# Performance work log

Hardware: AMD Instinct MI355X
Metric: run time of the kernel (lower is better)

The kernel has to match this reference:

```python
import jax, jax.numpy as jnp
import numpy as np

HEADS = 4
OUT_DIM = 64
NEG_SLOPE = 0.2


def setup_inputs() -> dict:
    key = jax.random.key(0)
    k1, k2, k3, k4 = jax.random.split(key, 4)
    n, in_dim = 4096, 256
    x = jax.random.normal(k1, (n, in_dim), dtype=jnp.float32)
    adj = jax.random.randint(k2, (n, n), 0, 2, dtype=jnp.int32)
    # lin: in_dim -> heads*out_dim (no bias), stored as [in_dim, heads*out_dim]
    W = jax.random.normal(k3, (in_dim, HEADS * OUT_DIM), dtype=jnp.float32) * 0.05
    # att_weight: [heads, 2*out_dim]
    att = jax.random.normal(k4, (HEADS, 2 * OUT_DIM), dtype=jnp.float32) * 0.05
    return {"x": x, "adj": adj, "W": W, "att": att}


def reference(x, adj, W, att):
    n = x.shape[0]
    h = (x @ W).reshape(n, HEADS, OUT_DIM)  # [n, H, D]
    # scores[i,j,h] = att[h] . cat(h_i, h_j) = <h_i, a_src[h]> + <h_j, a_dst[h]>
    a_src, a_dst = att[:, :OUT_DIM], att[:, OUT_DIM:]
    e_src = jnp.einsum('nhd,hd->nh', h, a_src)  # [n, H]
    e_dst = jnp.einsum('nhd,hd->nh', h, a_dst)  # [n, H]
    scores = e_src[:, None, :] + e_dst[None, :, :]  # [n, n, H]
    scores = jax.nn.leaky_relu(scores, negative_slope=NEG_SLOPE)
    mask = (adj > 0)[:, :, None]  # [n, n, 1]
    scores = jnp.where(mask, scores, -jnp.inf)
    alpha = jax.nn.softmax(scores, axis=1)  # softmax over neighbors j
    # h_prime[i,h,d] = sum_j alpha[i,j,h] * h[j,h,d]
    h_prime = jnp.einsum('ijh,jhd->ihd', alpha, h)
    return h_prime.reshape(n, HEADS * OUT_DIM)
```

## Files before the change

### kernel.cpp

```cpp
#include <hip/hip_runtime.h>
#include <hip/hip_bf16.h>

#define HEADS 4
#define ODIM 64
#define HD 256
#define NEG_SLOPE 0.2f

typedef __attribute__((ext_vector_type(8))) short bf16x8;
typedef __attribute__((ext_vector_type(4))) float floatx4;
typedef __attribute__((ext_vector_type(2))) float floatx2;

__global__ __launch_bounds__(256) void pack_xw(const float* __restrict__ x,
                                               const float* __restrict__ W,
                                               __hip_bfloat16* __restrict__ xh,
                                               __hip_bfloat16* __restrict__ xl,
                                               __hip_bfloat16* __restrict__ wh,
                                               __hip_bfloat16* __restrict__ wl,
                                               int K, int nxb) {
    const int b = blockIdx.x;
    const int Kc = K >> 5;
    if (b < nxb) {
        const int g = b * 256 + threadIdx.x;
        const int lane = g & 63, frag = g >> 6;
        const int kc = frag % Kc, mc = frag / Kc;
        const int l16 = lane & 15, q = lane >> 4;
        const float* src = x + (size_t)(mc * 16 + l16) * K + kc * 32 + q * 8;
        const float4 v0 = *(const float4*)src;
        const float4 v1 = *(const float4*)(src + 4);
        const float vv[8] = {v0.x, v0.y, v0.z, v0.w, v1.x, v1.y, v1.z, v1.w};
        union { __hip_bfloat16 b[8]; bf16x8 v; } H, L;
        #pragma unroll
        for (int p = 0; p < 8; ++p) {
            H.b[p] = __float2bfloat16(vv[p]);
            L.b[p] = __float2bfloat16(vv[p] - __bfloat162float(H.b[p]));
        }
        *(bf16x8*)&xh[(size_t)frag * 512 + lane * 8] = H.v;
        *(bf16x8*)&xl[(size_t)frag * 512 + lane * 8] = L.v;
    } else {
        const int g = (b - nxb) * 256 + threadIdx.x;
        const int lane = g & 63, frag = g >> 6;
        const int kc = frag % Kc, nc = frag / Kc;
        const int l16 = lane & 15, q = lane >> 4;
        union { __hip_bfloat16 b[8]; bf16x8 v; } H, L;
        #pragma unroll
        for (int p = 0; p < 8; ++p) {
            const float w = W[(size_t)(kc * 32 + q * 8 + p) * HD + nc * 16 + l16];
            H.b[p] = __float2bfloat16(w);
            L.b[p] = __float2bfloat16(w - __bfloat162float(H.b[p]));
        }
        *(bf16x8*)&wh[(size_t)frag * 512 + lane * 8] = H.v;
        *(bf16x8*)&wl[(size_t)frag * 512 + lane * 8] = L.v;
    }
}

__global__ __launch_bounds__(256) void gemm_fused(
    const __hip_bfloat16* __restrict__ xh, const __hip_bfloat16* __restrict__ xl,
    const __hip_bfloat16* __restrict__ wh, const __hip_bfloat16* __restrict__ wl,
    const float* __restrict__ att, float4* __restrict__ E4,
    __hip_bfloat16* __restrict__ hbB, int n, int K) {

    __shared__ __hip_bfloat16 T[64][80];

    const int tid = threadIdx.x, wave = tid >> 6, lane = tid & 63;
    const int q = lane >> 4, l16 = lane & 15;
    const int m0 = blockIdx.x * 64;
    const int head = blockIdx.y;
    const int Kc = K >> 5;
    const int mc = (m0 >> 4) + wave;

    floatx4 acc[4] = {{0.f,0.f,0.f,0.f},{0.f,0.f,0.f,0.f},{0.f,0.f,0.f,0.f},{0.f,0.f,0.f,0.f}};

    const __hip_bfloat16* Axh = xh + (size_t)mc * Kc * 512 + lane * 8;
    const __hip_bfloat16* Axl = xl + (size_t)mc * Kc * 512 + lane * 8;
    const __hip_bfloat16* Bwh = wh + lane * 8;
    const __hip_bfloat16* Bwl = wl + lane * 8;
    #pragma unroll 2
    for (int kc = 0; kc < Kc; ++kc) {
        const bf16x8 ah = *(const bf16x8*)(Axh + (size_t)kc * 512);
        const bf16x8 al = *(const bf16x8*)(Axl + (size_t)kc * 512);
        #pragma unroll
        for (int nt = 0; nt < 4; ++nt) {
            const size_t fo = (size_t)((head * 4 + nt) * Kc + kc) * 512;
            const bf16x8 bh = *(const bf16x8*)(Bwh + fo);
            const bf16x8 bl = *(const bf16x8*)(Bwl + fo);
            acc[nt] = __builtin_amdgcn_mfma_f32_16x16x32_bf16(ah, bh, acc[nt], 0, 0, 0);
            acc[nt] = __builtin_amdgcn_mfma_f32_16x16x32_bf16(ah, bl, acc[nt], 0, 0, 0);
            acc[nt] = __builtin_amdgcn_mfma_f32_16x16x32_bf16(al, bh, acc[nt], 0, 0, 0);
        }
    }

    float as_v[4], ad_v[4];
    #pragma unroll
    for (int nt = 0; nt < 4; ++nt) {
        as_v[nt] = att[head * 2 * ODIM + nt * 16 + l16];
        ad_v[nt] = att[head * 2 * ODIM + ODIM + nt * 16 + l16];
    }
    #pragma unroll
    for (int r = 0; r < 4; ++r) {
        float ps = 0.f, pd = 0.f;
        #pragma unroll
        for (int nt = 0; nt < 4; ++nt) {
            ps = fmaf(acc[nt][r], as_v[nt], ps);
            pd = fmaf(acc[nt][r], ad_v[nt], pd);
        }
        #pragma unroll
        for (int m = 1; m <= 8; m <<= 1) {
            ps += __shfl_xor(ps, m, 64);
            pd += __shfl_xor(pd, m, 64);
        }
        if (l16 == 0) {
            const int i = m0 + wave * 16 + q * 4 + r;
            E4[i * HEADS + head] = make_float4(__expf(ps), __expf(NEG_SLOPE * ps),
                                               __expf(pd), __expf(NEG_SLOPE * pd));
        }
    }

    #pragma unroll
    for (int nt = 0; nt < 4; ++nt) {
        union { __hip_bfloat16 b[4]; uint2 u; } pk;
        #pragma unroll
        for (int r = 0; r < 4; ++r) pk.b[r] = __float2bfloat16(acc[nt][r]);
        *(uint2*)&T[nt * 16 + l16][wave * 16 + q * 4] = pk.u;
    }
    __syncthreads();

    #pragma unroll
    for (int ffi = 0; ffi < 2; ++ffi) {
        const int ff = (tid >> 6) + ffi * 4;
        const int kcl = ff >> 2, nt = ff & 3;
        const bf16x8 v = *(const bf16x8*)&T[nt * 16 + l16][kcl * 32 + q * 8];
        const size_t frag = ((size_t)head * (n >> 5) + (m0 >> 5) + kcl) * 4 + nt;
        *(bf16x8*)&hbB[frag * 512 + lane * 8] = v;
    }
}

__global__ __launch_bounds__(256, 4) void aggregate(
    const int* __restrict__ adj, const float4* __restrict__ E4,
    const __hip_bfloat16* __restrict__ hbB, float* __restrict__ outsp,
    float* __restrict__ densp, int n, int KR) {

    __shared__ unsigned short adjL[2][32][72];
    __shared__ float2 EdL[2][HEADS][64];

    const int tid = threadIdx.x;
    const int wave = tid >> 6, lane = tid & 63;
    const int q = lane >> 4, l16 = lane & 15, q8 = (lane >> 4) * 8;
    const int i0 = blockIdx.x * 32;
    const int K0 = blockIdx.y * KR;

    const int sr = tid >> 3, sg = (tid & 7) * 8;
    const int je = tid >> 2, he = tid & 3;

    floatx2 es12[2];
    #pragma unroll
    for (int mt = 0; mt < 2; ++mt) {
        const float4 e = E4[(i0 + mt * 16 + l16) * HEADS + wave];
        es12[mt][0] = e.x; es12[mt][1] = e.y;
    }

    union { short s[8]; bf16x8 v; } bones;
    #pragma unroll
    for (int p = 0; p < 8; ++p) bones.s[p] = (l16 == 0) ? (short)0x3F80 : (short)0;

    floatx4 acc[2][4];
    floatx4 accd[2];
    #pragma unroll
    for (int mt = 0; mt < 2; ++mt) {
        accd[mt] = (floatx4){0.f, 0.f, 0.f, 0.f};
        #pragma unroll
        for (int nt = 0; nt < 4; ++nt) acc[mt][nt] = (floatx4){0.f, 0.f, 0.f, 0.f};
    }

    const int* aprow = &adj[(size_t)(i0 + sr) * n];

    int4 aj0, aj1; float4 ev;
    {
        const int* ap = aprow + K0 + sg;
        aj0 = *(const int4*)ap; aj1 = *(const int4*)(ap + 4);
        ev = E4[(K0 + je) * HEADS + he];
    }
    auto stage = [&](int buf) {
        const int av[8] = {aj0.x, aj0.y, aj0.z, aj0.w, aj1.x, aj1.y, aj1.z, aj1.w};
        uint4 u;
        u.x = (av[0] > 0 ? 0xFFFFu : 0u) | (av[1] > 0 ? 0xFFFF0000u : 0u);
        u.y = (av[2] > 0 ? 0xFFFFu : 0u) | (av[3] > 0 ? 0xFFFF0000u : 0u);
        u.z = (av[4] > 0 ? 0xFFFFu : 0u) | (av[5] > 0 ? 0xFFFF0000u : 0u);
        u.w = (av[6] > 0 ? 0xFFFFu : 0u) | (av[7] > 0 ? 0xFFFF0000u : 0u);
        *(uint4*)&adjL[buf][sr][sg] = u;
        EdL[buf][he][je] = make_float2(ev.z, ev.w);
    };
    stage(0);
    __syncthreads();

    int cur = 0;
    for (int jc = K0; jc < K0 + KR; jc += 64) {
        int jn = jc + 64; if (jn >= K0 + KR) jn = K0;
        {
            const int* ap = aprow + jn + sg;
            aj0 = *(const int4*)ap; aj1 = *(const int4*)(ap + 4);
            ev = E4[(jn + je) * HEADS + he];
        }

        const size_t kbase = ((size_t)wave * (n >> 5) + (jc >> 5)) * 4;
        #pragma unroll
        for (int ks = 0; ks < 2; ++ks) {
            bf16x8 bfr[4];
            #pragma unroll
            for (int nt = 0; nt < 4; ++nt)
                bfr[nt] = *(const bf16x8*)&hbB[(kbase + ks * 4 + nt) * 512 + lane * 8];

            const float4* ep = (const float4*)&EdL[cur][wave][ks * 32 + q8];
            const float4 e01 = ep[0], e23 = ep[1], e45 = ep[2], e67 = ep[3];
            floatx2 ed[8];
            ed[0][0]=e01.x; ed[0][1]=e01.y;  ed[1][0]=e01.z; ed[1][1]=e01.w;
            ed[2][0]=e23.x; ed[2][1]=e23.y;  ed[3][0]=e23.z; ed[3][1]=e23.w;
            ed[4][0]=e45.x; ed[4][1]=e45.y;  ed[5][0]=e45.z; ed[5][1]=e45.w;
            ed[6][0]=e67.x; ed[6][1]=e67.y;  ed[7][0]=e67.z; ed[7][1]=e67.w;

            #pragma unroll
            for (int mt = 0; mt < 2; ++mt) {
                const uint4 msk = *(const uint4*)&adjL[cur][mt * 16 + l16][ks * 32 + q8];
                const unsigned int mm[4] = {msk.x, msk.y, msk.z, msk.w};
                union { unsigned int u[4]; bf16x8 v; } af;
                #pragma unroll
                for (int p = 0; p < 4; ++p) {
                    const floatx2 pa = es12[mt] * ed[2 * p];
                    const floatx2 pb = es12[mt] * ed[2 * p + 1];
                    const float wa = fmaxf(pa[0], pa[1]);
                    const float wb = fmaxf(pb[0], pb[1]);
                    af.u[p] = __builtin_amdgcn_perm(__float_as_uint(wb), __float_as_uint(wa),
                                                    0x07060302u) & mm[p];
                }
                #pragma unroll
                for (int nt = 0; nt < 4; ++nt)
                    acc[mt][nt] = __builtin_amdgcn_mfma_f32_16x16x32_bf16(af.v, bfr[nt], acc[mt][nt], 0, 0, 0);
                accd[mt] = __builtin_amdgcn_mfma_f32_16x16x32_bf16(af.v, bones.v, accd[mt], 0, 0, 0);
            }
        }

        stage(cur ^ 1);
        __syncthreads();
        cur ^= 1;
    }

    const size_t sOut = (size_t)blockIdx.y * n * HD;
    #pragma unroll
    for (int mt = 0; mt < 2; ++mt)
        #pragma unroll
        for (int nt = 0; nt < 4; ++nt)
            #pragma unroll
            for (int r = 0; r < 4; ++r)
                outsp[sOut + (size_t)(i0 + mt * 16 + q * 4 + r) * HD + wave * ODIM + nt * 16 + l16] = acc[mt][nt][r];
    if (l16 == 0) {
        #pragma unroll
        for (int mt = 0; mt < 2; ++mt)
            #pragma unroll
            for (int r = 0; r < 4; ++r)
                densp[((size_t)blockIdx.y * n + i0 + mt * 16 + q * 4 + r) * HEADS + wave] = accd[mt][r];
    }
}

__global__ __launch_bounds__(256) void normalize(const float* __restrict__ outsp,
                                                 const float* __restrict__ densp,
                                                 float* __restrict__ out, int n, int splits) {
    const int g = blockIdx.x * 256 + threadIdx.x;
    const int i = g >> 6;
    const int c4 = (g & 63) * 4;
    const int head = c4 >> 6;
    float den = 0.f;
    for (int s = 0; s < splits; ++s) den += densp[((size_t)s * n + i) * HEADS + head];
    float4 v = {0.f, 0.f, 0.f, 0.f};
    for (int s = 0; s < splits; ++s) {
        const float4 t = *(const float4*)&outsp[(size_t)s * n * HD + (size_t)i * HD + c4];
        v.x += t.x; v.y += t.y; v.z += t.z; v.w += t.w;
    }
    const float inv = 1.0f / den;
    v.x *= inv; v.y *= inv; v.z *= inv; v.w *= inv;
    *(float4*)&out[(size_t)i * HD + c4] = v;
}

extern "C" void kernel_launch(void* const* d_in, const int* in_sizes, int n_in,
                              void* d_out, int out_size, void* d_ws, size_t ws_size,
                              hipStream_t stream) {
    const float* x   = (const float*)d_in[0];
    const int*   adj = (const int*)d_in[1];
    const float* W   = (const float*)d_in[2];
    const float* att = (const float*)d_in[3];
    float* out = (float*)d_out;

    const int in_dim = in_sizes[2] / HD;
    const int n = in_sizes[0] / in_dim;

    char* ws = (char*)d_ws;
    size_t off = 0;
    auto alloc = [&](size_t bytes) -> void* {
        void* p = ws + off; off += (bytes + 255) & ~(size_t)255; return p;
    };
    __hip_bfloat16* xh = (__hip_bfloat16*)alloc((size_t)n * in_dim * 2);
    __hip_bfloat16* xl = (__hip_bfloat16*)alloc((size_t)n * in_dim * 2);
    __hip_bfloat16* wh = (__hip_bfloat16*)alloc((size_t)in_dim * HD * 2);
    __hip_bfloat16* wl = (__hip_bfloat16*)alloc((size_t)in_dim * HD * 2);
    float4*         E4 = (float4*)alloc((size_t)n * HEADS * 16);
    __hip_bfloat16* hbB = (__hip_bfloat16*)alloc((size_t)n * HD * 2);

    const size_t outB = (size_t)n * HD * 4, denB = (size_t)n * HEADS * 4;
    int splits = 1;
    if      (ws_size >= off + 8 * (outB + denB)) splits = 8;
    else if (ws_size >= off + 4 * (outB + denB)) splits = 4;
    else if (ws_size >= off + 2 * (outB + denB)) splits = 2;
    float* densp = (float*)alloc((size_t)splits * denB);
    float* outsp = (splits == 1) ? out : (float*)alloc((size_t)splits * outB);

    const int nxb = (n / 16) * (in_dim / 32) * 64 / 256;
    const int nwb = (HD / 16) * (in_dim / 32) * 64 / 256;
    pack_xw<<<nxb + nwb, 256, 0, stream>>>(x, W, xh, xl, wh, wl, in_dim, nxb);
    gemm_fused<<<dim3(n / 64, HEADS), 256, 0, stream>>>(xh, xl, wh, wl, att, E4, hbB, n, in_dim);
    aggregate<<<dim3(n / 32, splits), 256, 0, stream>>>(adj, E4, hbB, outsp, densp, n, n / splits);
    normalize<<<n * 64 / 256, 256, 0, stream>>>(outsp, densp, out, n, splits);
}
```

Measured before the change: 147.4 us.

## Widen aggregate j-chunks to 128 with register double-prefetch and fixed 4 splits

After: 143.6 us. 2.6% less time.

```diff
diff --git a/kernel.cpp b/kernel.cpp
--- a/kernel.cpp
+++ b/kernel.cpp
@@ -5,6 +5,8 @@
 #define ODIM 64
 #define HD 256
 #define NEG_SLOPE 0.2f
+#define SPLITS 4
+#define BJ 128
 
 typedef __attribute__((ext_vector_type(8))) short bf16x8;
 typedef __attribute__((ext_vector_type(4))) float floatx4;
@@ -53,17 +55,17 @@
     }
 }
 
-__global__ __launch_bounds__(256) void gemm_fused(
+__global__ __launch_bounds__(128) void gemm_fused(
     const __hip_bfloat16* __restrict__ xh, const __hip_bfloat16* __restrict__ xl,
     const __hip_bfloat16* __restrict__ wh, const __hip_bfloat16* __restrict__ wl,
     const float* __restrict__ att, float4* __restrict__ E4,
     __hip_bfloat16* __restrict__ hbB, int n, int K) {
 
-    __shared__ __hip_bfloat16 T[64][80];
+    __shared__ __hip_bfloat16 T[64][40];
 
     const int tid = threadIdx.x, wave = tid >> 6, lane = tid & 63;
     const int q = lane >> 4, l16 = lane & 15;
-    const int m0 = blockIdx.x * 64;
+    const int m0 = blockIdx.x * 32;
     const int head = blockIdx.y;
     const int Kc = K >> 5;
     const int mc = (m0 >> 4) + wave;
@@ -78,15 +80,22 @@
     for (int kc = 0; kc < Kc; ++kc) {
         const bf16x8 ah = *(const bf16x8*)(Axh + (size_t)kc * 512);
         const bf16x8 al = *(const bf16x8*)(Axl + (size_t)kc * 512);
+        bf16x8 bh[4], bl[4];
         #pragma unroll
         for (int nt = 0; nt < 4; ++nt) {
             const size_t fo = (size_t)((head * 4 + nt) * Kc + kc) * 512;
-            const bf16x8 bh = *(const bf16x8*)(Bwh + fo);
-            const bf16x8 bl = *(const bf16x8*)(Bwl + fo);
-            acc[nt] = __builtin_amdgcn_mfma_f32_16x16x32_bf16(ah, bh, acc[nt], 0, 0, 0);
-            acc[nt] = __builtin_amdgcn_mfma_f32_16x16x32_bf16(ah, bl, acc[nt], 0, 0, 0);
-            acc[nt] = __builtin_amdgcn_mfma_f32_16x16x32_bf16(al, bh, acc[nt], 0, 0, 0);
-        }
+            bh[nt] = *(const bf16x8*)(Bwh + fo);
+            bl[nt] = *(const bf16x8*)(Bwl + fo);
+        }
+        #pragma unroll
+        for (int nt = 0; nt < 4; ++nt)
+            acc[nt] = __builtin_amdgcn_mfma_f32_16x16x32_bf16(ah, bh[nt], acc[nt], 0, 0, 0);
+        #pragma unroll
+        for (int nt = 0; nt < 4; ++nt)
+            acc[nt] = __builtin_amdgcn_mfma_f32_16x16x32_bf16(ah, bl[nt], acc[nt], 0, 0, 0);
+        #pragma unroll
+        for (int nt = 0; nt < 4; ++nt)
+            acc[nt] = __builtin_amdgcn_mfma_f32_16x16x32_bf16(al, bh[nt], acc[nt], 0, 0, 0);
     }
 
     float as_v[4], ad_v[4];
@@ -126,21 +135,20 @@
 
     #pragma unroll
     for (int ffi = 0; ffi < 2; ++ffi) {
-        const int ff = (tid >> 6) + ffi * 4;
-        const int kcl = ff >> 2, nt = ff & 3;
-        const bf16x8 v = *(const bf16x8*)&T[nt * 16 + l16][kcl * 32 + q * 8];
-        const size_t frag = ((size_t)head * (n >> 5) + (m0 >> 5) + kcl) * 4 + nt;
+        const int f = wave + ffi * 2;
+        const bf16x8 v = *(const bf16x8*)&T[f * 16 + l16][q * 8];
+        const size_t frag = ((size_t)head * (n >> 5) + (m0 >> 5)) * 4 + f;
         *(bf16x8*)&hbB[frag * 512 + lane * 8] = v;
     }
 }
 
-__global__ __launch_bounds__(256, 4) void aggregate(
+__global__ __launch_bounds__(256, 2) void aggregate(
     const int* __restrict__ adj, const float4* __restrict__ E4,
     const __hip_bfloat16* __restrict__ hbB, float* __restrict__ outsp,
     float* __restrict__ densp, int n, int KR) {
 
-    __shared__ unsigned short adjL[2][32][72];
-    __shared__ float2 EdL[2][HEADS][64];
+    __shared__ unsigned short adjL[2][32][136];
+    __shared__ float2 EdL[2][HEADS][BJ];
 
     const int tid = threadIdx.x;
     const int wave = tid >> 6, lane = tid & 63;
@@ -148,8 +156,8 @@
     const int i0 = blockIdx.x * 32;
     const int K0 = blockIdx.y * KR;
 
-    const int sr = tid >> 3, sg = (tid & 7) * 8;
-    const int je = tid >> 2, he = tid & 3;
+    const int sr = tid >> 3, sg = (tid & 7) * 16;
+    const int je = tid >> 1, heb = (tid & 1) * 2;
 
     floatx2 es12[2];
     #pragma unroll
@@ -172,54 +180,56 @@
     }
 
     const int* aprow = &adj[(size_t)(i0 + sr) * n];
-
-    int4 aj0, aj1; float4 ev;
-    {
-        const int* ap = aprow + K0 + sg;
-        aj0 = *(const int4*)ap; aj1 = *(const int4*)(ap + 4);
-        ev = E4[(K0 + je) * HEADS + he];
-    }
-    auto stage = [&](int buf) {
-        const int av[8] = {aj0.x, aj0.y, aj0.z, aj0.w, aj1.x, aj1.y, aj1.z, aj1.w};
-        uint4 u;
-        u.x = (av[0] > 0 ? 0xFFFFu : 0u) | (av[1] > 0 ? 0xFFFF0000u : 0u);
-        u.y = (av[2] > 0 ? 0xFFFFu : 0u) | (av[3] > 0 ? 0xFFFF0000u : 0u);
-        u.z = (av[4] > 0 ? 0xFFFFu : 0u) | (av[5] > 0 ? 0xFFFF0000u : 0u);
-        u.w = (av[6] > 0 ? 0xFFFFu : 0u) | (av[7] > 0 ? 0xFFFF0000u : 0u);
-        *(uint4*)&adjL[buf][sr][sg] = u;
-        EdL[buf][he][je] = make_float2(ev.z, ev.w);
+    const size_t fragbase = (size_t)wave * (n >> 5) * 4;
+
+    int4 ajA[4], ajB[4];
+    float4 evA0, evA1, evB0, evB1;
+
+    auto loadPref = [&](int jc, int4* aj, float4& e0, float4& e1) {
+        const int4* ap = (const int4*)(aprow + jc + sg);
+        aj[0] = ap[0]; aj[1] = ap[1]; aj[2] = ap[2]; aj[3] = ap[3];
+        e0 = E4[(jc + je) * HEADS + heb];
+        e1 = E4[(jc + je) * HEADS + heb + 1];
     };
-    stage(0);
-    __syncthreads();
-
-    int cur = 0;
-    for (int jc = K0; jc < K0 + KR; jc += 64) {
-        int jn = jc + 64; if (jn >= K0 + KR) jn = K0;
-        {
-            const int* ap = aprow + jn + sg;
-            aj0 = *(const int4*)ap; aj1 = *(const int4*)(ap + 4);
-            ev = E4[(jn + je) * HEADS + he];
-        }
-
-        const size_t kbase = ((size_t)wave * (n >> 5) + (jc >> 5)) * 4;
-        #pragma unroll
-        for (int ks = 0; ks < 2; ++ks) {
-            bf16x8 bfr[4];
-            #pragma unroll
-            for (int nt = 0; nt < 4; ++nt)
-                bfr[nt] = *(const bf16x8*)&hbB[(kbase + ks * 4 + nt) * 512 + lane * 8];
-
-            const float4* ep = (const float4*)&EdL[cur][wave][ks * 32 + q8];
+    auto stage = [&](int buf, const int4* aj, const float4& e0, const float4& e1) {
+        const int* av = (const int*)aj;
+        #pragma unroll
+        for (int g2 = 0; g2 < 2; ++g2) {
+            uint4 u;
+            u.x = (av[g2*8+0] > 0 ? 0xFFFFu : 0u) | (av[g2*8+1] > 0 ? 0xFFFF0000u : 0u);
+            u.y = (av[g2*8+2] > 0 ? 0xFFFFu : 0u) | (av[g2*8+3] > 0 ? 0xFFFF0000u : 0u);
+            u.z = (av[g2*8+4] > 0 ? 0xFFFFu : 0u) | (av[g2*8+5] > 0 ? 0xFFFF0000u : 0u);
+            u.w = (av[g2*8+6] > 0 ? 0xFFFFu : 0u) | (av[g2*8+7] > 0 ? 0xFFFF0000u : 0u);
+            *(uint4*)&adjL[buf][sr][sg + g2 * 8] = u;
+        }
+        EdL[buf][heb][je]     = make_float2(e0.z, e0.w);
+        EdL[buf][heb + 1][je] = make_float2(e1.z, e1.w);
+    };
+
+    auto computeChunk = [&](int buf, int jc) {
+        bf16x8 bA[4], bB[4];
+        #pragma unroll
+        for (int nt = 0; nt < 4; ++nt)
+            bA[nt] = *(const bf16x8*)&hbB[(fragbase + (size_t)(jc >> 5) * 4 + nt) * 512 + lane * 8];
+        #pragma unroll
+        for (int ks = 0; ks < 4; ++ks) {
+            const bf16x8* bcur = (ks & 1) ? bB : bA;
+            bf16x8* bnxt = (ks & 1) ? bA : bB;
+            if (ks < 3) {
+                #pragma unroll
+                for (int nt = 0; nt < 4; ++nt)
+                    bnxt[nt] = *(const bf16x8*)&hbB[(fragbase + (size_t)((jc >> 5) + ks + 1) * 4 + nt) * 512 + lane * 8];
+            }
+            const float4* ep = (const float4*)&EdL[buf][wave][ks * 32 + q8];
             const float4 e01 = ep[0], e23 = ep[1], e45 = ep[2], e67 = ep[3];
             floatx2 ed[8];
             ed[0][0]=e01.x; ed[0][1]=e01.y;  ed[1][0]=e01.z; ed[1][1]=e01.w;
             ed[2][0]=e23.x; ed[2][1]=e23.y;  ed[3][0]=e23.z; ed[3][1]=e23.w;
             ed[4][0]=e45.x; ed[4][1]=e45.y;  ed[5][0]=e45.z; ed[5][1]=e45.w;
             ed[6][0]=e67.x; ed[6][1]=e67.y;  ed[7][0]=e67.z; ed[7][1]=e67.w;
-
             #pragma unroll
             for (int mt = 0; mt < 2; ++mt) {
-                const uint4 msk = *(const uint4*)&adjL[cur][mt * 16 + l16][ks * 32 + q8];
+                const uint4 msk = *(const uint4*)&adjL[buf][mt * 16 + l16][ks * 32 + q8];
                 const unsigned int mm[4] = {msk.x, msk.y, msk.z, msk.w};
                 union { unsigned int u[4]; bf16x8 v; } af;
                 #pragma unroll
@@ -233,14 +243,30 @@
                 }
                 #pragma unroll
                 for (int nt = 0; nt < 4; ++nt)
-                    acc[mt][nt] = __builtin_amdgcn_mfma_f32_16x16x32_bf16(af.v, bfr[nt], acc[mt][nt], 0, 0, 0);
+                    acc[mt][nt] = __builtin_amdgcn_mfma_f32_16x16x32_bf16(af.v, bcur[nt], acc[mt][nt], 0, 0, 0);
                 accd[mt] = __builtin_amdgcn_mfma_f32_16x16x32_bf16(af.v, bones.v, accd[mt], 0, 0, 0);
             }
         }
-
-        stage(cur ^ 1);
+    };
+
+    const int KEND = K0 + KR;
+    loadPref(K0, ajA, evA0, evA1);
+    loadPref(K0 + BJ < KEND ? K0 + BJ : K0, ajB, evB0, evB1);
+    stage(0, ajA, evA0, evA1);
+    __syncthreads();
+
+    for (int jc = K0; jc < KEND; jc += 2 * BJ) {
+        int j2 = jc + 2 * BJ; if (j2 >= KEND) j2 = K0;
+        loadPref(j2, ajA, evA0, evA1);
+        computeChunk(0, jc);
+        stage(1, ajB, evB0, evB1);
         __syncthreads();
-        cur ^= 1;
+
+        int j3 = jc + 3 * BJ; if (j3 >= KEND) j3 = K0;
+        loadPref(j3, ajB, evB0, evB1);
+        computeChunk(1, jc + BJ);
+        stage(0, ajA, evA0, evA1);
+        __syncthreads();
     }
 
     const size_t sOut = (size_t)blockIdx.y * n * HD;
@@ -304,17 +330,13 @@
     __hip_bfloat16* hbB = (__hip_bfloat16*)alloc((size_t)n * HD * 2);
 
     const size_t outB = (size_t)n * HD * 4, denB = (size_t)n * HEADS * 4;
-    int splits = 1;
-    if      (ws_size >= off + 8 * (outB + denB)) splits = 8;
-    else if (ws_size >= off + 4 * (outB + denB)) splits = 4;
-    else if (ws_size >= off + 2 * (outB + denB)) splits = 2;
-    float* densp = (float*)alloc((size_t)splits * denB);
-    float* outsp = (splits == 1) ? out : (float*)alloc((size_t)splits * outB);
+    float* densp = (float*)alloc((size_t)SPLITS * denB);
+    float* outsp = (float*)alloc((size_t)SPLITS * outB);
 
     const int nxb = (n / 16) * (in_dim / 32) * 64 / 256;
     const int nwb = (HD / 16) * (in_dim / 32) * 64 / 256;
     pack_xw<<<nxb + nwb, 256, 0, stream>>>(x, W, xh, xl, wh, wl, in_dim, nxb);
-    gemm_fused<<<dim3(n / 64, HEADS), 256, 0, stream>>>(xh, xl, wh, wl, att, E4, hbB, n, in_dim);
-    aggregate<<<dim3(n / 32, splits), 256, 0, stream>>>(adj, E4, hbB, outsp, densp, n, n / splits);
-    normalize<<<n * 64 / 256, 256, 0, stream>>>(outsp, densp, out, n, splits);
-}
+    gemm_fused<<<dim3(n / 32, HEADS), 128, 0, stream>>>(xh, xl, wh, wl, att, E4, hbB, n, in_dim);
+    aggregate<<<dim3(n / 32, SPLITS), 256, 0, stream>>>(adj, E4, hbB, outsp, densp, n, n / SPLITS);
+    normalize<<<n * 64 / 256, 256, 0, stream>>>(outsp, densp, out, n, SPLITS);
+}
```
